# Optimization experiments

Measured on AMD Instinct MI355X. Metric: run time of the kernel, lower is better.

Reference implementation:

```python
import math
import jax
import jax.numpy as jnp
import numpy as np

B, T, D = 1, 2048, 1024
H, KV, DH = 16, 4, 64
E, TOPK, DFF = 32, 4, 1024
WINDOW = 128
EPS = 1e-5
ROPE_BASE = 150000.0
ROPE_SCALE = 32.0


def setup_inputs() -> dict:
    key = jax.random.key(0)
    ks = jax.random.split(key, 12)
    s = 0.02  # init scale for stability
    return {
        "x": jax.random.normal(ks[0], (B, T, D), jnp.float32),
        "attn_norm_w": 1.0 + 0.02 * jax.random.normal(ks[1], (D,), jnp.float32),
        "ffn_norm_w": 1.0 + 0.02 * jax.random.normal(ks[2], (D,), jnp.float32),
        "qkv_w": s * jax.random.normal(ks[3], (D, H * DH + 2 * KV * DH), jnp.float32),
        "qkv_b": s * jax.random.normal(ks[4], (H * DH + 2 * KV * DH,), jnp.float32),
        "proj_w": s * jax.random.normal(ks[5], (H * DH, D), jnp.float32),
        "proj_b": s * jax.random.normal(ks[6], (D,), jnp.float32),
        "attn_sink": 0.5 * jax.random.normal(ks[7], (H,), jnp.float32),
        "gate_w": s * jax.random.normal(ks[8], (D, E), jnp.float32),
        "gate_b": s * jax.random.normal(ks[9], (E,), jnp.float32),
        "W_up": s * jax.random.normal(ks[10], (E, D, 2 * DFF), jnp.float32),
        "W_down": s * jax.random.normal(ks[11], (E, DFF, D), jnp.float32),
    }


def _rmsnorm(x, w):
    rms = jax.lax.rsqrt(jnp.mean(x * x, axis=-1, keepdims=True) + EPS)
    return w * (x * rms)


def _apply_rope(x, sin, cos):
    # x: [B, h, T, dh]; sin/cos: [T, dh//2] -> interleaved rotation
    x1, x2 = x[..., ::2], x[..., 1::2]
    out = jnp.stack([x1 * cos - x2 * sin, x1 * sin + x2 * cos], axis=-1)
    return out.reshape(x.shape)


def reference(x, attn_norm_w, ffn_norm_w, qkv_w, qkv_b, proj_w, proj_b,
              attn_sink, gate_w, gate_b, W_up, W_down):
    Bx, Tx, Dx = x.shape
    # ---- attention branch ----
    h = _rmsnorm(x, attn_norm_w)
    qkv = h @ qkv_w + qkv_b
    q = qkv[..., : H * DH].reshape(Bx, Tx, H, DH).transpose(0, 2, 1, 3)
    k = qkv[..., H * DH : H * DH + KV * DH].reshape(Bx, Tx, KV, DH).transpose(0, 2, 1, 3)
    v = qkv[..., H * DH + KV * DH :].reshape(Bx, Tx, KV, DH).transpose(0, 2, 1, 3)
    # RoPE angles: pos/scale * base^{-2i/dh}
    pos = jnp.arange(Tx, dtype=jnp.float32) / ROPE_SCALE
    inv_freq = 1.0 / (ROPE_BASE ** (jnp.arange(0, DH, 2, dtype=jnp.float32) / DH))
    freqs = pos[:, None] * inv_freq[None, :]  # [T, DH//2]
    sin, cos = jnp.sin(freqs), jnp.cos(freqs)
    q = _apply_rope(q, sin, cos)
    k = _apply_rope(k, sin, cos)
    rep = H // KV
    k = jnp.repeat(k, rep, axis=1)
    v = jnp.repeat(v, rep, axis=1)
    logits = jnp.einsum('bhqd,bhkd->bhqk', q, k) / math.sqrt(DH)
    i = jnp.arange(Tx)[:, None]
    j = jnp.arange(Tx)[None, :]
    mask = (j > i) | (i - j > WINDOW)  # sliding-window causal
    logits = jnp.where(mask, -jnp.inf, logits)
    lse = jax.nn.logsumexp(logits, axis=-1, keepdims=True)  # [B,H,T,1]
    denom_log = jnp.logaddexp(lse, attn_sink.reshape(1, H, 1, 1))
    attn = jnp.exp(logits - denom_log)  # rows sum to < 1 due to sink
    y = jnp.einsum('bhqk,bhkd->bhqd', attn, v)
    y = y.transpose(0, 2, 1, 3).reshape(Bx, Tx, H * DH)
    x = x + (y @ proj_w + proj_b)
    # ---- token-choice MoE branch ----
    h2 = _rmsnorm(x, ffn_norm_w).reshape(Bx * Tx, Dx)
    glogits = h2 @ gate_w + gate_b  # [N, E]
    topv, topi = jax.lax.top_k(glogits, TOPK)
    gw = jax.nn.softmax(topv, axis=-1)  # [N, TOPK]
    N = Bx * Tx
    combine = jnp.zeros((N, E), x.dtype).at[jnp.arange(N)[:, None], topi].add(gw)
    def body(acc, we):
        wu, wd, ce = we  # [D,2DFF], [DFF,D], [N]
        ug = h2 @ wu
        u, g = ug[:, :DFF], ug[:, DFF:]
        return acc + ce[:, None] * ((jax.nn.silu(g) * u) @ wd), None
    y2, _ = jax.lax.scan(body, jnp.zeros_like(h2), (W_up, W_down, combine.T))
    return x + y2.reshape(Bx, Tx, Dx)
```

## Files before the change

### kernel.cpp

```cpp
#include <hip/hip_runtime.h>
#include <hip/hip_bf16.h>

#define NEx 32
#define QKVN 1536
#define MAXTILES 96

typedef __attribute__((ext_vector_type(4))) float f32x4_t;
typedef __attribute__((ext_vector_type(8))) __bf16 bf16x8_t;

__device__ __forceinline__ unsigned short f2bfu(float f) {
  union { float f; unsigned int u; } a; a.f = f;
  unsigned int r = a.u + 0x7fffu + ((a.u >> 16) & 1u);
  return (unsigned short)(r >> 16);
}
__device__ __forceinline__ float bf2f(unsigned short u) {
  union { unsigned int u; float f; } a; a.u = ((unsigned int)u) << 16; return a.f;
}
__device__ __forceinline__ uint2 pack4u(unsigned short a, unsigned short b,
                                        unsigned short c, unsigned short d) {
  return make_uint2((unsigned int)a | ((unsigned int)b << 16),
                    (unsigned int)c | ((unsigned int)d << 16));
}
__device__ __forceinline__ void split2(float v, unsigned short& hi, unsigned short& lo) {
  hi = f2bfu(v);
  lo = f2bfu(v - bf2f(hi));
}
typedef const __attribute__((address_space(1))) void* gas_t;
typedef __attribute__((address_space(3))) void* las_t;
__device__ __forceinline__ void gl16(const void* g, void* l) {
  __builtin_amdgcn_global_load_lds((gas_t)g, (las_t)l, 16, 0, 0);
}

template<int SPLIT>
__global__ __launch_bounds__(256) void k_wT(const float* __restrict__ in,
    unsigned short* __restrict__ outh, unsigned short* __restrict__ outl, int N) {
  __shared__ float T[64][68];
  int k0 = blockIdx.x * 64, n0 = blockIdx.y * 64, e = blockIdx.z;
  const float* src = in + (size_t)e * 1024 * N;
  int t = threadIdx.x;
  int rk = t >> 2, c4 = (t & 3) * 4;
#pragma unroll
  for (int j = 0; j < 4; ++j) {
    int col = c4 + j * 16;
    f32x4_t v = *(const f32x4_t*)(src + (size_t)(k0 + rk) * N + n0 + col);
    *(f32x4_t*)&T[rk][col] = v;
  }
  __syncthreads();
  int nn = t >> 2, kc0 = (t & 3) * 16;
  size_t orow = ((size_t)e * N + n0 + nn) * 1024 + k0;
#pragma unroll
  for (int j = 0; j < 2; ++j) {
    int kc = kc0 + j * 8;
    unsigned short hi[8], lo[8];
#pragma unroll
    for (int q = 0; q < 8; ++q) split2(T[kc + q][nn], hi[q], lo[q]);
    uint2 a = pack4u(hi[0], hi[1], hi[2], hi[3]);
    uint2 b = pack4u(hi[4], hi[5], hi[6], hi[7]);
    *(uint4*)(outh + orow + kc) = make_uint4(a.x, a.y, b.x, b.y);
    if (SPLIT) {
      uint2 c = pack4u(lo[0], lo[1], lo[2], lo[3]);
      uint2 d = pack4u(lo[4], lo[5], lo[6], lo[7]);
      *(uint4*)(outl + orow + kc) = make_uint4(c.x, c.y, d.x, d.y);
    }
  }
}

__global__ __launch_bounds__(256) void k_rmsnorm_s(const float* __restrict__ x,
    const float* __restrict__ w, unsigned short* __restrict__ ph, unsigned short* __restrict__ pl) {
  int row = blockIdx.x, tid = threadIdx.x;
  f32x4_t v = *(const f32x4_t*)(x + (size_t)row * 1024 + tid * 4);
  float ss = v.x * v.x + v.y * v.y + v.z * v.z + v.w * v.w;
#pragma unroll
  for (int o = 32; o > 0; o >>= 1) ss += __shfl_xor(ss, o);
  __shared__ float red[4];
  if ((tid & 63) == 0) red[tid >> 6] = ss;
  __syncthreads();
  float sc = rsqrtf((red[0] + red[1] + red[2] + red[3]) * (1.f / 1024.f) + 1e-5f);
  const float* wr = w + tid * 4;
  ushort4 h4, l4;
  split2(v.x * sc * wr[0], h4.x, l4.x);
  split2(v.y * sc * wr[1], h4.y, l4.y);
  split2(v.z * sc * wr[2], h4.z, l4.z);
  split2(v.w * sc * wr[3], h4.w, l4.w);
  *(ushort4*)(ph + (size_t)row * 1024 + tid * 4) = h4;
  *(ushort4*)(pl + (size_t)row * 1024 + tid * 4) = l4;
}

__global__ __launch_bounds__(256) void k_rmsnorm_f(const float* __restrict__ x,
    const float* __restrict__ w, float* __restrict__ outf, unsigned short* __restrict__ outb,
    float* __restrict__ out) {
  int row = blockIdx.x, tid = threadIdx.x;
  f32x4_t v = *(const f32x4_t*)(x + (size_t)row * 1024 + tid * 4);
  *(f32x4_t*)(out + (size_t)row * 1024 + tid * 4) = v;
  float ss = v.x * v.x + v.y * v.y + v.z * v.z + v.w * v.w;
#pragma unroll
  for (int o = 32; o > 0; o >>= 1) ss += __shfl_xor(ss, o);
  __shared__ float red[4];
  if ((tid & 63) == 0) red[tid >> 6] = ss;
  __syncthreads();
  float sc = rsqrtf((red[0] + red[1] + red[2] + red[3]) * (1.f / 1024.f) + 1e-5f);
  const float* wr = w + tid * 4;
  f32x4_t o4;
  o4.x = v.x * sc * wr[0]; o4.y = v.y * sc * wr[1];
  o4.z = v.z * sc * wr[2]; o4.w = v.w * sc * wr[3];
  *(f32x4_t*)(outf + (size_t)row * 1024 + tid * 4) = o4;
  ushort4 b4;
  b4.x = f2bfu(o4.x); b4.y = f2bfu(o4.y); b4.z = f2bfu(o4.z); b4.w = f2bfu(o4.w);
  *(ushort4*)(outb + (size_t)row * 1024 + tid * 4) = b4;
}

template<int RES>
__global__ __launch_bounds__(256) void k_gemm_s(
    const unsigned short* __restrict__ Ahg, const unsigned short* __restrict__ Alg,
    const unsigned short* __restrict__ BhT, const unsigned short* __restrict__ BlT,
    const float* __restrict__ bias, const float* __restrict__ res,
    float* __restrict__ C, int N) {
  __shared__ unsigned short Ah[64 * 32], Al[64 * 32], Bh[128 * 32], Bl[128 * 32];
  int tid = threadIdx.x, lane = tid & 63, w = tid >> 6;
  int m0 = blockIdx.y * 64, n0 = blockIdx.x * 128;
  int wm = (w >> 1) * 32, wn = (w & 1) * 64;
  int rl = lane >> 2, koff = (lane & 3) * 8;
  const unsigned short* agh = Ahg + (size_t)(m0 + w * 16 + rl) * 1024 + koff;
  const unsigned short* agl = Alg + (size_t)(m0 + w * 16 + rl) * 1024 + koff;
  const unsigned short* bgh0 = BhT + (size_t)(n0 + (w * 2 + 0) * 16 + rl) * 1024 + koff;
  const unsigned short* bgh1 = BhT + (size_t)(n0 + (w * 2 + 1) * 16 + rl) * 1024 + koff;
  const unsigned short* bgl0 = BlT + (size_t)(n0 + (w * 2 + 0) * 16 + rl) * 1024 + koff;
  const unsigned short* bgl1 = BlT + (size_t)(n0 + (w * 2 + 1) * 16 + rl) * 1024 + koff;
  f32x4_t acc[2][4];
#pragma unroll
  for (int i = 0; i < 2; ++i)
#pragma unroll
    for (int j = 0; j < 4; ++j) acc[i][j] = (f32x4_t){0.f, 0.f, 0.f, 0.f};
  int fr = lane & 15, fc = (lane >> 4) * 8;
  for (int k0 = 0; k0 < 1024; k0 += 32) {
    gl16(agh + k0, (char*)Ah + w * 1024);
    gl16(agl + k0, (char*)Al + w * 1024);
    gl16(bgh0 + k0, (char*)Bh + (w * 2 + 0) * 1024);
    gl16(bgh1 + k0, (char*)Bh + (w * 2 + 1) * 1024);
    gl16(bgl0 + k0, (char*)Bl + (w * 2 + 0) * 1024);
    gl16(bgl1 + k0, (char*)Bl + (w * 2 + 1) * 1024);
    __syncthreads();
    bf16x8_t fah[2], fal[2], fbh[4], fbl[4];
#pragma unroll
    for (int mi = 0; mi < 2; ++mi) {
      fah[mi] = *(const bf16x8_t*)(Ah + (wm + mi * 16 + fr) * 32 + fc);
      fal[mi] = *(const bf16x8_t*)(Al + (wm + mi * 16 + fr) * 32 + fc);
    }
#pragma unroll
    for (int nj = 0; nj < 4; ++nj) {
      fbh[nj] = *(const bf16x8_t*)(Bh + (wn + nj * 16 + fr) * 32 + fc);
      fbl[nj] = *(const bf16x8_t*)(Bl + (wn + nj * 16 + fr) * 32 + fc);
    }
#pragma unroll
    for (int mi = 0; mi < 2; ++mi)
#pragma unroll
      for (int nj = 0; nj < 4; ++nj) {
        acc[mi][nj] = __builtin_amdgcn_mfma_f32_16x16x32_bf16(fah[mi], fbh[nj], acc[mi][nj], 0, 0, 0);
        acc[mi][nj] = __builtin_amdgcn_mfma_f32_16x16x32_bf16(fah[mi], fbl[nj], acc[mi][nj], 0, 0, 0);
        acc[mi][nj] = __builtin_amdgcn_mfma_f32_16x16x32_bf16(fal[mi], fbh[nj], acc[mi][nj], 0, 0, 0);
      }
    __syncthreads();
  }
  int frow = (lane >> 4) * 4;
#pragma unroll
  for (int mi = 0; mi < 2; ++mi)
#pragma unroll
    for (int nj = 0; nj < 4; ++nj) {
      int col = n0 + wn + nj * 16 + fr;
      float bv = bias[col];
#pragma unroll
      for (int r = 0; r < 4; ++r) {
        int row = m0 + wm + mi * 16 + frow + r;
        float v = acc[mi][nj][r] + bv;
        if (RES) v += res[(size_t)row * N + col];
        C[(size_t)row * N + col] = v;
      }
    }
}

__global__ __launch_bounds__(256) void k_rope(float* __restrict__ qkv) {
  int idx = blockIdx.x * 256 + threadIdx.x;
  int i = idx & 31;
  int r5 = idx >> 5;
  int hd = r5 % 20, t = r5 / 20;
  int col = (hd < 16) ? hd * 64 : 1024 + (hd - 16) * 64;
  float* p = qkv + (size_t)t * QKVN + col + 2 * i;
  float2 v = *(float2*)p;
  float invf = exp2f(-(float)i * (17.194602975157967f / 32.f));
  float ang = ((float)t * (1.f / 32.f)) * invf;
  float s, c;
  sincosf(ang, &s, &c);
  float2 o; o.x = v.x * c - v.y * s; o.y = v.x * s + v.y * c;
  *(float2*)p = o;
}

__global__ __launch_bounds__(256) void k_attn(const float* __restrict__ qkv,
    const float* __restrict__ sink, unsigned short* __restrict__ yh,
    unsigned short* __restrict__ yl) {
  __shared__ float Kl[72 * 65];
  __shared__ float Vl[72 * 64];
  __shared__ float ql[16][64];
  __shared__ float pl[4][4][128];
  int i0 = blockIdx.x * 16, hh = blockIdx.y;
  int g = hh >> 2;
  int jb = i0 - 128; if (jb < 0) jb = 0;
  int nk = i0 + 16 - jb;
  int tid = threadIdx.x, wid = tid >> 6, lane = tid & 63;
  {
    int r = tid >> 4, d4 = (tid & 15) * 4;
    *(f32x4_t*)&ql[r][d4] = *(const f32x4_t*)(qkv + (size_t)(i0 + r) * QKVN + hh * 64 + d4);
  }
  float sk = sink[hh];
  float m_[4], s_[4], y_[4];
#pragma unroll
  for (int qq = 0; qq < 4; ++qq) { m_[qq] = sk; s_[qq] = 0.f; y_[qq] = 0.f; }
  int nch = (nk + 71) / 72;
  int cbase = 0;
  int qb = wid * 4;
  for (int ch = 0; ch < nch; ++ch) {
    int csz = nk - cbase; if (csz > 72) csz = 72;
    __syncthreads();
    for (int id = tid; id < csz * 16; id += 256) {
      int c = id >> 4, d4 = (id & 15) * 4;
      const float* kp = qkv + (size_t)(jb + cbase + c) * QKVN + 1024 + g * 64 + d4;
      *(f32x4_t*)&Kl[c * 65 + d4] = *(const f32x4_t*)kp;
      *(f32x4_t*)&Vl[c * 64 + d4] = *(const f32x4_t*)(kp + 256);
    }
    __syncthreads();
    int s1 = lane + 64;
    int r1 = (s1 < csz) ? s1 : (csz - 1);
    const float* k0p = Kl + lane * 65;
    const float* k1p = Kl + r1 * 65;
    float a0[4] = {0.f, 0.f, 0.f, 0.f}, a1[4] = {0.f, 0.f, 0.f, 0.f};
#pragma unroll 4
    for (int d = 0; d < 64; ++d) {
      float k0 = k0p[d], k1 = k1p[d];
#pragma unroll
      for (int qq = 0; qq < 4; ++qq) {
        float qd = ql[qb + qq][d];
        a0[qq] += qd * k0;
        a1[qq] += qd * k1;
      }
    }
    int c0 = cbase + lane, c1 = cbase + s1;
    float fac_[4];
#pragma unroll
    for (int qq = 0; qq < 4; ++qq) {
      int cm = i0 + qb + qq - jb;
      bool ok0 = (lane < csz) && (c0 <= cm) && (c0 >= cm - 128);
      bool ok1 = (s1 < csz) && (c1 <= cm) && (c1 >= cm - 128);
      float l0 = ok0 ? a0[qq] * 0.125f : -1e30f;
      float l1 = ok1 ? a1[qq] * 0.125f : -1e30f;
      float mc = fmaxf(l0, l1);
#pragma unroll
      for (int o = 32; o > 0; o >>= 1) mc = fmaxf(mc, __shfl_xor(mc, o));
      float mo = m_[qq];
      float mn = fmaxf(mo, mc);
      float fac = __expf(mo - mn);
      float p0 = __expf(l0 - mn), p1 = __expf(l1 - mn);
      float ps = p0 + p1;
#pragma unroll
      for (int o = 32; o > 0; o >>= 1) ps += __shfl_xor(ps, o);
      m_[qq] = mn;
      s_[qq] = s_[qq] * fac + ps;
      pl[wid][qq][lane] = p0;
      pl[wid][qq][s1] = p1;
      fac_[qq] = fac;
    }
#pragma unroll
    for (int qq = 0; qq < 4; ++qq) y_[qq] *= fac_[qq];
    for (int s = 0; s < csz; ++s) {
      float v = Vl[s * 64 + lane];
      y_[0] += pl[wid][0][s] * v;
      y_[1] += pl[wid][1][s] * v;
      y_[2] += pl[wid][2][s] * v;
      y_[3] += pl[wid][3][s] * v;
    }
    cbase += csz;
  }
#pragma unroll
  for (int qq = 0; qq < 4; ++qq) {
    float inv = 1.f / (s_[qq] + __expf(sk - m_[qq]));
    int i = i0 + qb + qq;
    unsigned short hi, lo;
    split2(y_[qq] * inv, hi, lo);
    yh[(size_t)i * 1024 + hh * 64 + lane] = hi;
    yl[(size_t)i * 1024 + hh * 64 + lane] = lo;
  }
}

__global__ __launch_bounds__(64) void k_gate(const float* __restrict__ h2f,
    const float* __restrict__ gw, const float* __restrict__ gb,
    int* __restrict__ texp, float* __restrict__ twt) {
  int t = blockIdx.x, l = threadIdx.x;
  int e = l & 31, half = l >> 5;
  const float* hr = h2f + (size_t)t * 1024 + half * 512;
  const float* wp = gw + (size_t)half * 512 * 32 + e;
  float s = 0;
  for (int d = 0; d < 512; ++d) s += hr[d] * wp[(size_t)d * 32];
  s += __shfl_xor(s, 32);
  __shared__ float gl[32];
  if (l < 32) gl[l] = s + gb[e];
  __syncthreads();
  if (l == 0) {
    int bi[4]; float bv[4];
    for (int j = 0; j < 4; ++j) {
      int mi_ = 0; float mv = gl[0];
      for (int q = 1; q < 32; ++q) if (gl[q] > mv) { mv = gl[q]; mi_ = q; }
      bi[j] = mi_; bv[j] = mv; gl[mi_] = -1e30f;
    }
    float mx = bv[0], sum = 0, wv[4];
    for (int j = 0; j < 4; ++j) { wv[j] = __expf(bv[j] - mx); sum += wv[j]; }
    float inv = 1.f / sum;
    for (int j = 0; j < 4; ++j) { texp[t * 4 + j] = bi[j]; twt[t * 4 + j] = wv[j] * inv; }
  }
}

__global__ __launch_bounds__(256) void k_moe_count(const int* __restrict__ texp, int* __restrict__ cnt) {
  int e = blockIdx.x, tid = threadIdx.x;
  int c = 0;
  for (int i = tid; i < 8192; i += 256) c += (texp[i] == e);
#pragma unroll
  for (int o = 32; o > 0; o >>= 1) c += __shfl_xor(c, o);
  __shared__ int red[4];
  if ((tid & 63) == 0) red[tid >> 6] = c;
  __syncthreads();
  if (tid == 0) cnt[e] = red[0] + red[1] + red[2] + red[3];
}

__global__ void k_moe_off(const int* __restrict__ cnt, int* __restrict__ off,
                          int* __restrict__ tiles) {
  if (threadIdx.x == 0) {
    int s = 0, t = 0;
    for (int e = 0; e < NEx; ++e) {
      off[e] = s;
      int nt = (cnt[e] + 127) >> 7;
      for (int j = 0; j < nt; ++j) tiles[t++] = e | (j << 8);
      s += cnt[e];
    }
    for (; t < MAXTILES; ++t) tiles[t] = -1;
  }
}

__global__ __launch_bounds__(256) void k_moe_assign(const int* __restrict__ texp,
    const float* __restrict__ twt, const int* __restrict__ off,
    int* __restrict__ slot_token, float* __restrict__ slot_wt) {
  int e = blockIdx.x, tid = threadIdx.x;
  int b0 = tid * 32;
  int c = 0;
  for (int i = 0; i < 32; ++i) c += (texp[b0 + i] == e);
  __shared__ int pre[256];
  pre[tid] = c;
  __syncthreads();
  for (int d = 1; d < 256; d <<= 1) {
    int v = (tid >= d) ? pre[tid - d] : 0;
    __syncthreads();
    pre[tid] += v;
    __syncthreads();
  }
  int run = off[e] + pre[tid] - c;
  for (int i = 0; i < 32; ++i) {
    int idx = b0 + i;
    if (texp[idx] == e) {
      slot_token[run] = idx >> 2;
      slot_wt[run] = twt[idx];
      ++run;
    }
  }
}

__global__ __launch_bounds__(256) void k_moe_up(const unsigned short* __restrict__ h2b,
    const unsigned short* __restrict__ WupT, const int* __restrict__ cnt,
    const int* __restrict__ off, const int* __restrict__ tiles,
    const int* __restrict__ slot_token, unsigned short* __restrict__ act) {
  int code = tiles[blockIdx.y];
  if (code < 0) return;
  int e = code & 255;
  int m0 = (code >> 8) << 7;
  int ne = cnt[e];
  int n0 = blockIdx.x * 64;
  int base = off[e];
  __shared__ unsigned short Asm[128 * 32];
  __shared__ unsigned short Bsm[128 * 32];
  int tid = threadIdx.x, lane = tid & 63, w = tid >> 6;
  int rl = lane >> 2, koff = (lane & 3) * 8;
  const unsigned short* ag[2];
  const unsigned short* bg[2];
#pragma unroll
  for (int i = 0; i < 2; ++i) {
    int row = (w * 2 + i) * 16 + rl;
    int tok = (m0 + row < ne) ? slot_token[base + m0 + row] : 0;
    ag[i] = h2b + (size_t)tok * 1024 + koff;
    int grow = (row < 64) ? (n0 + row) : (1024 + n0 + row - 64);
    bg[i] = WupT + (size_t)e * 2048 * 1024 + (size_t)grow * 1024 + koff;
  }
  f32x4_t acc[2][8];
#pragma unroll
  for (int i = 0; i < 2; ++i)
#pragma unroll
    for (int j = 0; j < 8; ++j) acc[i][j] = (f32x4_t){0.f, 0.f, 0.f, 0.f};
  int fr = lane & 15, fc = (lane >> 4) * 8;
  for (int k0 = 0; k0 < 1024; k0 += 32) {
    gl16(ag[0] + k0, (char*)Asm + (w * 2 + 0) * 1024);
    gl16(ag[1] + k0, (char*)Asm + (w * 2 + 1) * 1024);
    gl16(bg[0] + k0, (char*)Bsm + (w * 2 + 0) * 1024);
    gl16(bg[1] + k0, (char*)Bsm + (w * 2 + 1) * 1024);
    __syncthreads();
    bf16x8_t af[2], bfr[8];
#pragma unroll
    for (int mi = 0; mi < 2; ++mi)
      af[mi] = *(const bf16x8_t*)(Asm + (w * 32 + mi * 16 + fr) * 32 + fc);
#pragma unroll
    for (int nj = 0; nj < 8; ++nj)
      bfr[nj] = *(const bf16x8_t*)(Bsm + (nj * 16 + fr) * 32 + fc);
#pragma unroll
    for (int mi = 0; mi < 2; ++mi)
#pragma unroll
      for (int nj = 0; nj < 8; ++nj)
        acc[mi][nj] = __builtin_amdgcn_mfma_f32_16x16x32_bf16(af[mi], bfr[nj], acc[mi][nj], 0, 0, 0);
    __syncthreads();
  }
  int frow = (lane >> 4) * 4;
#pragma unroll
  for (int mi = 0; mi < 2; ++mi)
#pragma unroll
    for (int r = 0; r < 4; ++r) {
      int row = m0 + w * 32 + mi * 16 + frow + r;
      if (row < ne) {
#pragma unroll
        for (int nj = 0; nj < 4; ++nj) {
          float u = acc[mi][nj][r];
          float gg = acc[mi][nj + 4][r];
          float sig = 1.f / (1.f + __expf(-gg));
          act[(size_t)(base + row) * 1024 + n0 + nj * 16 + fr] = f2bfu(u * gg * sig);
        }
      }
    }
}

__global__ __launch_bounds__(256) void k_moe_down(const unsigned short* __restrict__ act,
    const unsigned short* __restrict__ WdnT, const int* __restrict__ cnt,
    const int* __restrict__ off, const int* __restrict__ tiles,
    const int* __restrict__ slot_token, const float* __restrict__ slot_wt,
    float* __restrict__ out) {
  int code = tiles[blockIdx.y];
  if (code < 0) return;
  int e = code & 255;
  int m0 = (code >> 8) << 7;
  int ne = cnt[e];
  int n0 = blockIdx.x * 128;
  int base = off[e];
  __shared__ unsigned short Asm[128 * 32];
  __shared__ unsigned short Bsm[128 * 32];
  int tid = threadIdx.x, lane = tid & 63, w = tid >> 6;
  int wm = (w >> 1) * 64, wn = (w & 1) * 64;
  int rl = lane >> 2, koff = (lane & 3) * 8;
  const unsigned short* ag[2];
  const unsigned short* bg[2];
#pragma unroll
  for (int i = 0; i < 2; ++i) {
    int row = (w * 2 + i) * 16 + rl;
    ag[i] = act + (size_t)(base + m0 + row) * 1024 + koff;
    bg[i] = WdnT + (size_t)e * 1024 * 1024 + (size_t)(n0 + row) * 1024 + koff;
  }
  f32x4_t acc[4][4];
#pragma unroll
  for (int i = 0; i < 4; ++i)
#pragma unroll
    for (int j = 0; j < 4; ++j) acc[i][j] = (f32x4_t){0.f, 0.f, 0.f, 0.f};
  int fr = lane & 15, fc = (lane >> 4) * 8;
  for (int k0 = 0; k0 < 1024; k0 += 32) {
    gl16(ag[0] + k0, (char*)Asm + (w * 2 + 0) * 1024);
    gl16(ag[1] + k0, (char*)Asm + (w * 2 + 1) * 1024);
    gl16(bg[0] + k0, (char*)Bsm + (w * 2 + 0) * 1024);
    gl16(bg[1] + k0, (char*)Bsm + (w * 2 + 1) * 1024);
    __syncthreads();
    bf16x8_t af[4], bfr[4];
#pragma unroll
    for (int mi = 0; mi < 4; ++mi)
      af[mi] = *(const bf16x8_t*)(Asm + (wm + mi * 16 + fr) * 32 + fc);
#pragma unroll
    for (int nj = 0; nj < 4; ++nj)
      bfr[nj] = *(const bf16x8_t*)(Bsm + (wn + nj * 16 + fr) * 32 + fc);
#pragma unroll
    for (int mi = 0; mi < 4; ++mi)
#pragma unroll
      for (int nj = 0; nj < 4; ++nj)
        acc[mi][nj] = __builtin_amdgcn_mfma_f32_16x16x32_bf16(af[mi], bfr[nj], acc[mi][nj], 0, 0, 0);
    __syncthreads();
  }
  int frow = (lane >> 4) * 4;
#pragma unroll
  for (int mi = 0; mi < 4; ++mi)
#pragma unroll
    for (int r = 0; r < 4; ++r) {
      int row = m0 + wm + mi * 16 + frow + r;
      if (row < ne) {
        int slot = base + row;
        int token = slot_token[slot];
        float wt = slot_wt[slot];
#pragma unroll
        for (int nj = 0; nj < 4; ++nj) {
          int col = n0 + wn + nj * 16 + fr;
          atomicAdd(&out[(size_t)token * 1024 + col], wt * acc[mi][nj][r]);
        }
      }
    }
}

extern "C" void kernel_launch(void* const* d_in, const int* in_sizes, int n_in,
                              void* d_out, int out_size, void* d_ws, size_t ws_size,
                              hipStream_t stream) {
  const float* x           = (const float*)d_in[0];
  const float* attn_norm_w = (const float*)d_in[1];
  const float* ffn_norm_w  = (const float*)d_in[2];
  const float* qkv_w       = (const float*)d_in[3];
  const float* qkv_b       = (const float*)d_in[4];
  const float* proj_w      = (const float*)d_in[5];
  const float* proj_b      = (const float*)d_in[6];
  const float* attn_sink   = (const float*)d_in[7];
  const float* gate_w      = (const float*)d_in[8];
  const float* gate_b      = (const float*)d_in[9];
  const float* W_up        = (const float*)d_in[10];
  const float* W_down      = (const float*)d_in[11];
  float* out = (float*)d_out;

  char* ws = (char*)d_ws;
  size_t o = 0;
  auto alloc = [&](size_t bytes) -> void* {
    void* p = ws + o;
    o = (o + bytes + 255) & ~(size_t)255;
    return p;
  };
  unsigned short* WT      = (unsigned short*)alloc((size_t)32 * 2048 * 1024 * 2);
  unsigned short* qkvThi  = (unsigned short*)alloc((size_t)1536 * 1024 * 2);
  unsigned short* qkvTlo  = (unsigned short*)alloc((size_t)1536 * 1024 * 2);
  unsigned short* projThi = (unsigned short*)alloc((size_t)1024 * 1024 * 2);
  unsigned short* projTlo = (unsigned short*)alloc((size_t)1024 * 1024 * 2);
  unsigned short* pAhi    = (unsigned short*)alloc((size_t)2048 * 1024 * 2);
  unsigned short* pAlo    = (unsigned short*)alloc((size_t)2048 * 1024 * 2);
  float* qkv              = (float*)alloc((size_t)2048 * 1536 * 4);
  float* x1               = (float*)alloc((size_t)2048 * 1024 * 4);
  unsigned short* act     = (unsigned short*)alloc((size_t)(8192 + 128) * 1024 * 2);
  int* texp               = (int*)alloc(8192 * 4);
  float* twt              = (float*)alloc(8192 * 4);
  int* cnt                = (int*)alloc(256);
  int* offs               = (int*)alloc(256);
  int* tiles              = (int*)alloc(MAXTILES * 4);
  int* slot_token         = (int*)alloc(8192 * 4);
  float* slot_wt          = (float*)alloc(8192 * 4);
  float* h2f              = qkv;
  unsigned short* h2b     = (unsigned short*)(qkv + (size_t)2048 * 1024);

  k_wT<1><<<dim3(16, 24, 1), 256, 0, stream>>>(qkv_w, qkvThi, qkvTlo, 1536);
  k_wT<1><<<dim3(16, 16, 1), 256, 0, stream>>>(proj_w, projThi, projTlo, 1024);
  k_wT<0><<<dim3(16, 32, 32), 256, 0, stream>>>(W_up, WT, nullptr, 2048);

  k_rmsnorm_s<<<2048, 256, 0, stream>>>(x, attn_norm_w, pAhi, pAlo);
  k_gemm_s<0><<<dim3(12, 32), 256, 0, stream>>>(pAhi, pAlo, qkvThi, qkvTlo, qkv_b, nullptr, qkv, 1536);
  k_rope<<<5120, 256, 0, stream>>>(qkv);
  k_attn<<<dim3(128, 16), 256, 0, stream>>>(qkv, attn_sink, pAhi, pAlo);
  k_gemm_s<1><<<dim3(8, 32), 256, 0, stream>>>(pAhi, pAlo, projThi, projTlo, proj_b, x, x1, 1024);
  k_rmsnorm_f<<<2048, 256, 0, stream>>>(x1, ffn_norm_w, h2f, h2b, out);
  k_gate<<<2048, 64, 0, stream>>>(h2f, gate_w, gate_b, texp, twt);
  k_moe_count<<<32, 256, 0, stream>>>(texp, cnt);
  k_moe_off<<<1, 64, 0, stream>>>(cnt, offs, tiles);
  k_moe_assign<<<32, 256, 0, stream>>>(texp, twt, offs, slot_token, slot_wt);
  k_moe_up<<<dim3(16, MAXTILES), 256, 0, stream>>>(h2b, WT, cnt, offs, tiles, slot_token, act);
  k_wT<0><<<dim3(16, 16, 32), 256, 0, stream>>>(W_down, WT, nullptr, 1024);
  k_moe_down<<<dim3(8, MAXTILES), 256, 0, stream>>>(act, WT, cnt, offs, tiles, slot_token, slot_wt, out);
}
```

Baseline: 433.5 us.

## Fuse RoPE into attention via sin/cos table and count experts in gate

Removes the standalone RoPE kernel. A small sin/cos table is precomputed once, and the rotation is applied to Q and K as they are loaded into shared memory inside the attention kernel. Expert counting also moves into the gate kernel through atomicAdd, with the counters zeroed in rmsnorm, so the separate count kernel is gone. The cost is K being re-rotated by every head block that loads it, plus atomic contention on 32 counters.

```diff
diff --git a/kernel.cpp b/kernel.cpp
--- a/kernel.cpp
+++ b/kernel.cpp
@@ -29,6 +29,18 @@
 typedef __attribute__((address_space(3))) void* las_t;
 __device__ __forceinline__ void gl16(const void* g, void* l) {
   __builtin_amdgcn_global_load_lds((gas_t)g, (las_t)l, 16, 0, 0);
+}
+
+__global__ __launch_bounds__(256) void k_ropetab(float* __restrict__ cost,
+    float* __restrict__ sint) {
+  int idx = blockIdx.x * 256 + threadIdx.x;
+  int i = idx & 31, t = idx >> 5;
+  float invf = exp2f(-(float)i * (17.194602975157967f / 32.f));
+  float ang = ((float)t * (1.f / 32.f)) * invf;
+  float s, c;
+  sincosf(ang, &s, &c);
+  cost[idx] = c;
+  sint[idx] = s;
 }
 
 template<int SPLIT>
@@ -88,8 +100,9 @@
 
 __global__ __launch_bounds__(256) void k_rmsnorm_f(const float* __restrict__ x,
     const float* __restrict__ w, float* __restrict__ outf, unsigned short* __restrict__ outb,
-    float* __restrict__ out) {
+    float* __restrict__ out, int* __restrict__ cnt) {
   int row = blockIdx.x, tid = threadIdx.x;
+  if (row == 0 && tid < NEx) cnt[tid] = 0;
   f32x4_t v = *(const f32x4_t*)(x + (size_t)row * 1024 + tid * 4);
   *(f32x4_t*)(out + (size_t)row * 1024 + tid * 4) = v;
   float ss = v.x * v.x + v.y * v.y + v.z * v.z + v.w * v.w;
@@ -178,23 +191,8 @@
     }
 }
 
-__global__ __launch_bounds__(256) void k_rope(float* __restrict__ qkv) {
-  int idx = blockIdx.x * 256 + threadIdx.x;
-  int i = idx & 31;
-  int r5 = idx >> 5;
-  int hd = r5 % 20, t = r5 / 20;
-  int col = (hd < 16) ? hd * 64 : 1024 + (hd - 16) * 64;
-  float* p = qkv + (size_t)t * QKVN + col + 2 * i;
-  float2 v = *(float2*)p;
-  float invf = exp2f(-(float)i * (17.194602975157967f / 32.f));
-  float ang = ((float)t * (1.f / 32.f)) * invf;
-  float s, c;
-  sincosf(ang, &s, &c);
-  float2 o; o.x = v.x * c - v.y * s; o.y = v.x * s + v.y * c;
-  *(float2*)p = o;
-}
-
 __global__ __launch_bounds__(256) void k_attn(const float* __restrict__ qkv,
+    const float* __restrict__ cost, const float* __restrict__ sint,
     const float* __restrict__ sink, unsigned short* __restrict__ yh,
     unsigned short* __restrict__ yl) {
   __shared__ float Kl[72 * 65];
@@ -208,7 +206,14 @@
   int tid = threadIdx.x, wid = tid >> 6, lane = tid & 63;
   {
     int r = tid >> 4, d4 = (tid & 15) * 4;
-    *(f32x4_t*)&ql[r][d4] = *(const f32x4_t*)(qkv + (size_t)(i0 + r) * QKVN + hh * 64 + d4);
+    int t = i0 + r;
+    f32x4_t qv = *(const f32x4_t*)(qkv + (size_t)t * QKVN + hh * 64 + d4);
+    float2 cs = *(const float2*)&cost[t * 32 + (d4 >> 1)];
+    float2 sn = *(const float2*)&sint[t * 32 + (d4 >> 1)];
+    f32x4_t qr;
+    qr.x = qv.x * cs.x - qv.y * sn.x; qr.y = qv.x * sn.x + qv.y * cs.x;
+    qr.z = qv.z * cs.y - qv.w * sn.y; qr.w = qv.z * sn.y + qv.w * cs.y;
+    *(f32x4_t*)&ql[r][d4] = qr;
   }
   float sk = sink[hh];
   float m_[4], s_[4], y_[4];
@@ -222,8 +227,15 @@
     __syncthreads();
     for (int id = tid; id < csz * 16; id += 256) {
       int c = id >> 4, d4 = (id & 15) * 4;
-      const float* kp = qkv + (size_t)(jb + cbase + c) * QKVN + 1024 + g * 64 + d4;
-      *(f32x4_t*)&Kl[c * 65 + d4] = *(const f32x4_t*)kp;
+      int t = jb + cbase + c;
+      const float* kp = qkv + (size_t)t * QKVN + 1024 + g * 64 + d4;
+      f32x4_t kv = *(const f32x4_t*)kp;
+      float2 cs = *(const float2*)&cost[t * 32 + (d4 >> 1)];
+      float2 sn = *(const float2*)&sint[t * 32 + (d4 >> 1)];
+      f32x4_t kr;
+      kr.x = kv.x * cs.x - kv.y * sn.x; kr.y = kv.x * sn.x + kv.y * cs.x;
+      kr.z = kv.z * cs.y - kv.w * sn.y; kr.w = kv.z * sn.y + kv.w * cs.y;
+      *(f32x4_t*)&Kl[c * 65 + d4] = kr;
       *(f32x4_t*)&Vl[c * 64 + d4] = *(const f32x4_t*)(kp + 256);
     }
     __syncthreads();
@@ -291,7 +303,7 @@
 
 __global__ __launch_bounds__(64) void k_gate(const float* __restrict__ h2f,
     const float* __restrict__ gw, const float* __restrict__ gb,
-    int* __restrict__ texp, float* __restrict__ twt) {
+    int* __restrict__ texp, float* __restrict__ twt, int* __restrict__ cnt) {
   int t = blockIdx.x, l = threadIdx.x;
   int e = l & 31, half = l >> 5;
   const float* hr = h2f + (size_t)t * 1024 + half * 512;
@@ -312,20 +324,12 @@
     float mx = bv[0], sum = 0, wv[4];
     for (int j = 0; j < 4; ++j) { wv[j] = __expf(bv[j] - mx); sum += wv[j]; }
     float inv = 1.f / sum;
-    for (int j = 0; j < 4; ++j) { texp[t * 4 + j] = bi[j]; twt[t * 4 + j] = wv[j] * inv; }
-  }
-}
-
-__global__ __launch_bounds__(256) void k_moe_count(const int* __restrict__ texp, int* __restrict__ cnt) {
-  int e = blockIdx.x, tid = threadIdx.x;
-  int c = 0;
-  for (int i = tid; i < 8192; i += 256) c += (texp[i] == e);
-#pragma unroll
-  for (int o = 32; o > 0; o >>= 1) c += __shfl_xor(c, o);
-  __shared__ int red[4];
-  if ((tid & 63) == 0) red[tid >> 6] = c;
-  __syncthreads();
-  if (tid == 0) cnt[e] = red[0] + red[1] + red[2] + red[3];
+    for (int j = 0; j < 4; ++j) {
+      texp[t * 4 + j] = bi[j];
+      twt[t * 4 + j] = wv[j] * inv;
+      atomicAdd(&cnt[bi[j]], 1);
+    }
+  }
 }
 
 __global__ void k_moe_off(const int* __restrict__ cnt, int* __restrict__ off,
@@ -542,6 +546,8 @@
   float* qkv              = (float*)alloc((size_t)2048 * 1536 * 4);
   float* x1               = (float*)alloc((size_t)2048 * 1024 * 4);
   unsigned short* act     = (unsigned short*)alloc((size_t)(8192 + 128) * 1024 * 2);
+  float* cost             = (float*)alloc((size_t)2048 * 32 * 4);
+  float* sint             = (float*)alloc((size_t)2048 * 32 * 4);
   int* texp               = (int*)alloc(8192 * 4);
   float* twt              = (float*)alloc(8192 * 4);
   int* cnt                = (int*)alloc(256);
@@ -552,18 +558,17 @@
   float* h2f              = qkv;
   unsigned short* h2b     = (unsigned short*)(qkv + (size_t)2048 * 1024);
 
+  k_ropetab<<<256, 256, 0, stream>>>(cost, sint);
   k_wT<1><<<dim3(16, 24, 1), 256, 0, stream>>>(qkv_w, qkvThi, qkvTlo, 1536);
   k_wT<1><<<dim3(16, 16, 1), 256, 0, stream>>>(proj_w, projThi, projTlo, 1024);
   k_wT<0><<<dim3(16, 32, 32), 256, 0, stream>>>(W_up, WT, nullptr, 2048);
 
   k_rmsnorm_s<<<2048, 256, 0, stream>>>(x, attn_norm_w, pAhi, pAlo);
   k_gemm_s<0><<<dim3(12, 32), 256, 0, stream>>>(pAhi, pAlo, qkvThi, qkvTlo, qkv_b, nullptr, qkv, 1536);
-  k_rope<<<5120, 256, 0, stream>>>(qkv);
-  k_attn<<<dim3(128, 16), 256, 0, stream>>>(qkv, attn_sink, pAhi, pAlo);
+  k_attn<<<dim3(128, 16), 256, 0, stream>>>(qkv, cost, sint, attn_sink, pAhi, pAlo);
   k_gemm_s<1><<<dim3(8, 32), 256, 0, stream>>>(pAhi, pAlo, projThi, projTlo, proj_b, x, x1, 1024);
-  k_rmsnorm_f<<<2048, 256, 0, stream>>>(x1, ffn_norm_w, h2f, h2b, out);
-  k_gate<<<2048, 64, 0, stream>>>(h2f, gate_w, gate_b, texp, twt);
-  k_moe_count<<<32, 256, 0, stream>>>(texp, cnt);
+  k_rmsnorm_f<<<2048, 256, 0, stream>>>(x1, ffn_norm_w, h2f, h2b, out, cnt);
+  k_gate<<<2048, 64, 0, stream>>>(h2f, gate_w, gate_b, texp, twt, cnt);
   k_moe_off<<<1, 64, 0, stream>>>(cnt, offs, tiles);
   k_moe_assign<<<32, 256, 0, stream>>>(texp, twt, offs, slot_token, slot_wt);
   k_moe_up<<<dim3(16, MAXTILES), 256, 0, stream>>>(h2b, WT, cnt, offs, tiles, slot_token, act);
```

After: 474.4 us. 1.09x slower.
